# Performance work log

Measured on AMD Instinct MI355X. Metric: run time of the kernel, lower is better.

## Reference

```python
import jax, jax.numpy as jnp
import numpy as np

B, S, E, NH = 2, 2048, 512, 4
DH = E // NH  # 128
KSZ = 4      # causal conv kernel size


def setup_inputs() -> dict:
    key = jax.random.key(0)
    ks = jax.random.split(key, 12)
    hw_std = (2.0 / 5.0 / DH) ** 0.5
    return {
        "x": jax.random.normal(ks[0], (B, S, E), jnp.float32),
        "W_up": jax.random.normal(ks[1], (2 * E, E), jnp.float32) * 0.02,
        "Wq": jax.random.normal(ks[2], (NH, DH, DH), jnp.float32) * hw_std,
        "Wk": jax.random.normal(ks[3], (NH, DH, DH), jnp.float32) * hw_std,
        "Wv": jax.random.normal(ks[4], (NH, DH, DH), jnp.float32) * hw_std,
        "conv_w": jax.random.normal(ks[5], (E, E, KSZ), jnp.float32) * (1.0 / (E * KSZ) ** 0.5),
        "conv_b": jnp.zeros((E,), jnp.float32),
        "Wi": jax.random.normal(ks[6], (NH, 3 * E), jnp.float32) * 0.01,
        "bi": jax.random.normal(ks[7], (NH,), jnp.float32) * 0.1,
        "Wf": jax.random.normal(ks[8], (NH, 3 * E), jnp.float32) * 0.01,
        "bf": jax.random.normal(ks[9], (NH,), jnp.float32),
        "skip": jnp.ones((E,), jnp.float32),
        "W_down": jax.random.normal(ks[10], (E, E), jnp.float32) * 0.02,
        "b_down": jnp.zeros((E,), jnp.float32),
    }


def _headwise(u, W):
    # LinearHeadwiseExpand: x -> [B,S,NH,dh] @ [NH,od,dh]
    b, s, e = u.shape
    nh = W.shape[0]
    uh = u.reshape(b, s, nh, -1)
    return jnp.einsum('bshd,hod->bsho', uh, W).reshape(b, s, e)


def reference(x, W_up, Wq, Wk, Wv, conv_w, conv_b, Wi, bi, Wf, bf, skip, W_down, b_down):
    b, s, e = x.shape
    nh = Wq.shape[0]
    dh = e // nh
    eps = 1e-6

    x_inner = x @ W_up.T                        # [B,S,2E]
    x_mlstm, z = jnp.split(x_inner, 2, axis=-1)

    # causal conv1d: left-pad kernel_size-1, trim implicit via padding spec
    xc = jnp.transpose(x_mlstm, (0, 2, 1))      # [B,E,S]
    conv = jax.lax.conv_general_dilated(
        xc, conv_w, window_strides=(1,), padding=[(KSZ - 1, 0)],
        dimension_numbers=('NCH', 'OIH', 'NCH')) + conv_b[None, :, None]
    x_conv_act = jax.nn.silu(jnp.transpose(conv, (0, 2, 1)))  # [B,S,E]

    q = _headwise(x_conv_act, Wq)
    k = _headwise(x_conv_act, Wk)
    v = _headwise(x_mlstm, Wv)

    gate_in = jnp.concatenate([q, k, v], axis=-1)           # [B,S,3E]
    igate = jnp.transpose(gate_in @ Wi.T + bi, (0, 2, 1))   # [B,NH,S]
    fgate = jnp.transpose(gate_in @ Wf.T + bf, (0, 2, 1))   # [B,NH,S]

    qh = jnp.transpose(q.reshape(b, s, nh, dh), (0, 2, 1, 3))  # [B,NH,S,DH]
    kh = jnp.transpose(k.reshape(b, s, nh, dh), (0, 2, 1, 3))
    vh = jnp.transpose(v.reshape(b, s, nh, dh), (0, 2, 1, 3))

    # log-space cumulative forget-gate D matrix
    log_fg = jax.nn.log_sigmoid(fgate)                      # [B,NH,S]
    lfc = jnp.cumsum(log_fg, axis=-1)                       # [B,NH,S]
    log_fg_mat = lfc[..., :, None] - lfc[..., None, :]      # [B,NH,S,S]
    mask = jnp.tril(jnp.ones((s, s), bool))
    log_fg_mat = jnp.where(mask, log_fg_mat, -jnp.inf)
    log_D = log_fg_mat + igate[..., None, :]                # + igate[j]

    max_log_D = jnp.max(log_D, axis=-1, keepdims=True)      # rowwise stabilize
    Dm = jnp.exp(log_D - max_log_D)

    qk = jnp.einsum('bhsd,bhtd->bhst', qh, kh) / (dh ** 0.5)
    C = qk * Dm
    normalizer = jnp.maximum(jnp.abs(jnp.sum(C, axis=-1, keepdims=True)),
                             jnp.exp(-max_log_D))
    Cn = C / (normalizer + eps)
    h = jnp.einsum('bhst,bhtd->bhsd', Cn, vh)               # [B,NH,S,DH]

    # MultiHeadLayerNorm = group_norm(num_groups=NH, no affine, eps=1e-5)
    ht = jnp.transpose(h, (0, 2, 1, 3))                     # [B,S,NH,DH]
    mean = jnp.mean(ht, axis=-1, keepdims=True)
    var = jnp.var(ht, axis=-1, keepdims=True)
    h_norm = ((ht - mean) / jnp.sqrt(var + 1e-5)).reshape(b, s, e)

    h_skip = h_norm + skip * x_conv_act
    h_state = h_skip * jax.nn.silu(z)
    return h_state @ W_down.T + b_down
```

## Files before the change

### kernel.cpp

```cpp
#include <hip/hip_runtime.h>
#include <hip/hip_bf16.h>
#include <math.h>

typedef __hip_bfloat16 bf16;
typedef unsigned short ushort_t;
typedef __bf16 v8bf __attribute__((ext_vector_type(8)));
typedef float v4f __attribute__((ext_vector_type(4)));

#define B_   2
#define S_   2048
#define E_   512
#define NH_  4
#define DH_  128
#define NIN_ 14
#define NSPLIT_ 4

__device__ inline ushort_t f2bf(float f) {
  union { float f; unsigned u; } v; v.f = f;
  unsigned r = (v.u + 0x7FFFu + ((v.u >> 16) & 1u)) >> 16;
  return (ushort_t)r;
}
__device__ inline float bf2f(ushort_t u) {
  union { unsigned uu; float ff; } c; c.uu = (unsigned)u << 16; return c.ff;
}

struct CvtArgs {
  const void* src[NIN_];
  float* dst[NIN_];
  ushort_t* bdst[NIN_];
  int sz[NIN_];
};

__global__ __launch_bounds__(256) void convert_all(CvtArgs a, const unsigned* modew) {
  const bool isbf = (*modew == 0x3F803F80u);
  const int t = blockIdx.y;
  const int n = a.sz[t];
  const int base = blockIdx.x * 1024 + threadIdx.x;
  const float* sf = (const float*)a.src[t];
  const bf16*  sb = (const bf16*)a.src[t];
  const ushort_t* su = (const ushort_t*)a.src[t];
  float* d = a.dst[t];
  ushort_t* bd = a.bdst[t];
#pragma unroll
  for (int k = 0; k < 4; ++k) {
    int idx = base + k * 256;
    if (idx < n) {
      float f = isbf ? __bfloat162float(sb[idx]) : sf[idx];
      if (d)  d[idx] = f;
      if (bd) bd[idx] = isbf ? su[idx] : f2bf(f);
    }
  }
}

__global__ __launch_bounds__(256) void conv_repack(
    const void* __restrict__ src, ushort_t* __restrict__ Wt, const unsigned* __restrict__ modew)
{
  const bool isbf = (*modew == 0x3F803F80u);
  int idx = blockIdx.x * 256 + threadIdx.x;
  if (idx < E_ * E_ * 4) {
    int k = idx & 3, i = (idx >> 2) & (E_ - 1), o = idx >> 11;
    ushort_t v;
    if (isbf) v = ((const ushort_t*)src)[idx];
    else      v = f2bf(((const float*)src)[idx]);
    Wt[((size_t)k * E_ + o) * E_ + i] = v;
  }
}

__global__ __launch_bounds__(256) void gates_repack(
    const void* __restrict__ wi, const void* __restrict__ wf,
    ushort_t* __restrict__ Wgh, ushort_t* __restrict__ Wgl,
    const unsigned* __restrict__ modew)
{
  const bool isbf = (*modew == 0x3F803F80u);
  int idx = blockIdx.x * 256 + threadIdx.x;
  if (idx < 16 * 3 * E_) {
    int row = idx / (3 * E_), col = idx % (3 * E_);
    float w = 0.f;
    if (row < 4)      w = isbf ? bf2f(((const ushort_t*)wi)[row * 3 * E_ + col])
                               : ((const float*)wi)[row * 3 * E_ + col];
    else if (row < 8) w = isbf ? bf2f(((const ushort_t*)wf)[(row - 4) * 3 * E_ + col])
                               : ((const float*)wf)[(row - 4) * 3 * E_ + col];
    ushort_t hi = f2bf(w);
    Wgh[idx] = hi;
    Wgl[idx] = f2bf(w - bf2f(hi));
  }
}

template <int NT, bool HAS_BIAS, bool OUT_BF16, bool OUT_LO, bool OUT_DUAL>
__global__ __launch_bounds__(128, 4) void gemm2(
    const ushort_t* __restrict__ A, int lda,
    const ushort_t* __restrict__ Bm, int ldb,
    const float* __restrict__ bias,
    ushort_t* __restrict__ Cb, ushort_t* __restrict__ Cl,
    void* __restrict__ Cd, int ldc,
    int M, int K, const unsigned* __restrict__ modew)
{
  const int nm = M >> 6;
  const int m0 = (blockIdx.x % nm) << 6;
  const int n0 = (blockIdx.x / nm) * (NT * 16);
  const int tid = threadIdx.x;
  const int wv = tid >> 6, lane = tid & 63;
  const int ln15 = lane & 15, quad = lane >> 4;
  const int mA = m0 + wv * 16 + ln15;
  const int mB = mA + 32;
  v4f accA[NT], accB[NT];
#pragma unroll
  for (int i = 0; i < NT; ++i) { accA[i] = (v4f){0,0,0,0}; accB[i] = (v4f){0,0,0,0}; }
  const ushort_t* arowA = A + (size_t)mA * lda + quad * 8;
  const ushort_t* arowB = A + (size_t)mB * lda + quad * 8;
  const ushort_t* brow = Bm + (size_t)(n0 + ln15) * ldb + quad * 8;
  for (int k0 = 0; k0 < K; k0 += 32) {
    v8bf aA = *(const v8bf*)(arowA + k0);
    v8bf aB = *(const v8bf*)(arowB + k0);
#pragma unroll
    for (int nt = 0; nt < NT; ++nt) {
      v8bf b = *(const v8bf*)(brow + (size_t)nt * 16 * ldb + k0);
      accA[nt] = __builtin_amdgcn_mfma_f32_16x16x32_bf16(aA, b, accA[nt], 0, 0, 0);
      accB[nt] = __builtin_amdgcn_mfma_f32_16x16x32_bf16(aB, b, accB[nt], 0, 0, 0);
    }
  }
  bool obf = false;
  if (OUT_DUAL) obf = (*modew == 0x3F803F80u);
#pragma unroll
  for (int half = 0; half < 2; ++half) {
    const v4f* acc = half ? accB : accA;
#pragma unroll
    for (int nt = 0; nt < NT; ++nt) {
#pragma unroll
      for (int rr = 0; rr < 4; ++rr) {
        int m = m0 + wv * 16 + half * 32 + quad * 4 + rr;
        int n = n0 + nt * 16 + ln15;
        float c = acc[nt][rr];
        if (HAS_BIAS) c += bias[n];
        size_t off = (size_t)m * ldc + n;
        if (OUT_BF16) {
          ushort_t hi = f2bf(c);
          Cb[off] = hi;
          if (OUT_LO) Cl[off] = f2bf(c - bf2f(hi));
        }
        if (OUT_DUAL) {
          if (obf) ((bf16*)Cd)[off] = __float2bfloat16(c);
          else     ((float*)Cd)[off] = c;
        }
      }
    }
  }
}

__global__ __launch_bounds__(256, 2) void conv_lds2(
    const ushort_t* __restrict__ xhi,
    const ushort_t* __restrict__ xlo,
    const ushort_t* __restrict__ Wt,
    const float* __restrict__ cb,
    float* __restrict__ xca,
    ushort_t* __restrict__ xcab)
{
  const int m0 = (blockIdx.x & 63) << 6;
  const int n0 = (blockIdx.x >> 6) << 6;
  const int tid = threadIdx.x;
  const int wv = tid >> 6;
  const int lane = tid & 63;
  const int ln15 = lane & 15, quad = lane >> 4;
  const bool boundary = (m0 & (S_ - 1)) == 0;

  constexpr int LP = 132;
  __shared__ ushort_t Ab[2][68 * LP];

  int srow[17], scol[17], sstr[17];
#pragma unroll
  for (int j = 0; j < 17; ++j) {
    int idx = j * 256 + tid;
    sstr[j] = idx / 2176;
    int rem = idx - sstr[j] * 2176;
    srow[j] = rem >> 5;
    scol[j] = (rem & 31) << 2;
  }
  ushort4 sreg[17];
  auto stage_load = [&](int c) {
#pragma unroll
    for (int j = 0; j < 17; ++j) {
      const ushort_t* src = sstr[j] ? xlo : xhi;
      sreg[j] = *(const ushort4*)(src + (ptrdiff_t)(m0 - 4 + srow[j]) * (2 * E_)
                                  + c * 128 + scol[j]);
    }
    if (boundary) {
#pragma unroll
      for (int j = 0; j < 17; ++j)
        if (srow[j] < 4) sreg[j] = make_ushort4(0, 0, 0, 0);
    }
  };
  auto stage_write = [&]() {
#pragma unroll
    for (int j = 0; j < 17; ++j)
      *(ushort4*)&Ab[sstr[j]][srow[j] * LP + scol[j]] = sreg[j];
  };

  v4f acc[4];
#pragma unroll
  for (int i = 0; i < 4; ++i) acc[i] = (v4f){0, 0, 0, 0};

  v8bf breg[16];
  auto loadB = [&](int c) {
    const ushort_t* bw = Wt + (size_t)(n0 + wv * 16 + ln15) * E_ + c * 128 + quad * 8;
#pragma unroll
    for (int t = 0; t < 4; ++t)
#pragma unroll
      for (int k0 = 0; k0 < 4; ++k0)
        breg[t * 4 + k0] = *(const v8bf*)(bw + (size_t)t * E_ * E_ + k0 * 32);
  };
  auto compute = [&]() {
#pragma unroll
    for (int t = 0; t < 4; ++t) {
#pragma unroll
      for (int k0 = 0; k0 < 4; ++k0) {
#pragma unroll
        for (int rt = 0; rt < 4; ++rt) {
          const int ro = (rt * 16 + ln15 + t + 1) * LP + k0 * 32 + quad * 8;
          v8bf a1 = *(const v8bf*)&Ab[0][ro];
          v8bf a2 = *(const v8bf*)&Ab[1][ro];
          acc[rt] = __builtin_amdgcn_mfma_f32_16x16x32_bf16(a1, breg[t * 4 + k0], acc[rt], 0, 0, 0);
          acc[rt] = __builtin_amdgcn_mfma_f32_16x16x32_bf16(a2, breg[t * 4 + k0], acc[rt], 0, 0, 0);
        }
      }
    }
  };

  stage_load(0);
  stage_write();
  __syncthreads();
#pragma unroll
  for (int c = 0; c < 4; ++c) {
    if (c < 3) stage_load(c + 1);
    loadB(c);
    compute();
    if (c < 3) {
      __syncthreads();
      stage_write();
      __syncthreads();
    }
  }

  const int col = n0 + wv * 16 + ln15;
  const float cbv = cb[col];
#pragma unroll
  for (int rt = 0; rt < 4; ++rt) {
#pragma unroll
    for (int rr = 0; rr < 4; ++rr) {
      const int row = m0 + rt * 16 + quad * 4 + rr;
      float c = acc[rt][rr] + cbv;
      float r = c / (1.f + __expf(-c));
      const size_t off = (size_t)row * E_ + col;
      xca[off] = r;
      xcab[off] = f2bf(r);
    }
  }
}

__global__ __launch_bounds__(256) void qkv_mfma(
    const ushort_t* __restrict__ xcab,
    const ushort_t* __restrict__ xmb,
    const ushort_t* __restrict__ wqb, const ushort_t* __restrict__ wkb, const ushort_t* __restrict__ wvb,
    ushort_t* __restrict__ qb, ushort_t* __restrict__ kb, ushort_t* __restrict__ vb,
    ushort_t* __restrict__ vtb)
{
  const int type = blockIdx.y >> 2;
  const int h = blockIdx.y & 3;
  const int m0 = blockIdx.x << 6;
  const int tid = threadIdx.x;
  const int wv = tid >> 6, lane = tid & 63;
  const int ln15 = lane & 15, quad = lane >> 4;

  const ushort_t* Asrc = (type == 2) ? (xmb + h * DH_) : (xcab + h * DH_);
  const int lda = (type == 2) ? (2 * E_) : E_;
  const ushort_t* W = ((type == 0) ? wqb : (type == 1) ? wkb : wvb) + (size_t)h * DH_ * DH_;
  ushort_t* dst = (type == 0) ? qb : (type == 1) ? kb : vb;

  v4f acc[8];
#pragma unroll
  for (int i = 0; i < 8; ++i) acc[i] = (v4f){0.f, 0.f, 0.f, 0.f};

  const ushort_t* arow = Asrc + (size_t)(m0 + wv * 16 + ln15) * lda + quad * 8;
  const ushort_t* brow = W + (size_t)ln15 * DH_ + quad * 8;
#pragma unroll
  for (int c = 0; c < 4; ++c) {
    v8bf a = *(const v8bf*)(arow + c * 32);
#pragma unroll
    for (int nt = 0; nt < 8; ++nt) {
      v8bf b = *(const v8bf*)(brow + (size_t)nt * 16 * DH_ + c * 32);
      acc[nt] = __builtin_amdgcn_mfma_f32_16x16x32_bf16(a, b, acc[nt], 0, 0, 0);
    }
  }
  const int bb = m0 >> 11;
  const int s0 = (m0 & (S_ - 1)) + wv * 16 + quad * 4;
#pragma unroll
  for (int nt = 0; nt < 8; ++nt) {
    ushort_t pk[4];
#pragma unroll
    for (int rr = 0; rr < 4; ++rr) {
      int m = m0 + wv * 16 + quad * 4 + rr;
      int s = m & (S_ - 1);
      int n = nt * 16 + ln15;
      ushort_t u = f2bf(acc[nt][rr]);
      pk[rr] = u;
      dst[((size_t)(bb * NH_ + h) * S_ + s) * DH_ + n] = u;
    }
    if (type == 2) {
      *(ushort4*)&vtb[((size_t)(bb * NH_ + h) * DH_ + nt * 16 + ln15) * S_ + s0] =
          make_ushort4(pk[0], pk[1], pk[2], pk[3]);
    }
  }
}

__global__ __launch_bounds__(64) void gates_mfma(
    const ushort_t* __restrict__ qb, const ushort_t* __restrict__ kb, const ushort_t* __restrict__ vb,
    const ushort_t* __restrict__ Wgh, const ushort_t* __restrict__ Wgl,
    const float* __restrict__ bi, const float* __restrict__ bfp,
    float* __restrict__ ig, float* __restrict__ fgo)
{
  const int m0 = blockIdx.x << 4;
  const int lane = threadIdx.x;
  const int ln15 = lane & 15, quad = lane >> 4;
  const int m = m0 + ln15;
  const int b = m >> 11, s = m & (S_ - 1);
  const size_t base0 = ((size_t)(b * NH_) * S_ + s) * DH_;

  v4f acc = (v4f){0.f, 0.f, 0.f, 0.f};
  const ushort_t* wh = Wgh + (size_t)ln15 * (3 * E_) + quad * 8;
  const ushort_t* wl = Wgl + (size_t)ln15 * (3 * E_) + quad * 8;
#pragma unroll
  for (int kk = 0; kk < 48; ++kk) {
    const int kg = kk * 32 + quad * 8;
    const int type = kg >> 9;
    const int h = (kg >> 7) & 3;
    const int d = kg & 127;
    const ushort_t* src = (type == 0) ? qb : (type == 1) ? kb : vb;
    v8bf a = *(const v8bf*)(src + base0 + (size_t)h * S_ * DH_ + d);
    v8bf bh2 = *(const v8bf*)(wh + kk * 32);
    v8bf bl2 = *(const v8bf*)(wl + kk * 32);
    acc = __builtin_amdgcn_mfma_f32_16x16x32_bf16(a, bh2, acc, 0, 0, 0);
    acc = __builtin_amdgcn_mfma_f32_16x16x32_bf16(a, bl2, acc, 0, 0, 0);
  }
  if (ln15 < 8) {
#pragma unroll
    for (int r = 0; r < 4; ++r) {
      int mm = m0 + quad * 4 + r;
      int bb2 = mm >> 11, ss = mm & (S_ - 1);
      if (ln15 < 4) ig [((size_t)(bb2 * NH_ + ln15)) * S_ + ss]       = acc[r] + bi[ln15];
      else          fgo[((size_t)(bb2 * NH_ + (ln15 - 4))) * S_ + ss] = acc[r] + bfp[ln15 - 4];
    }
  }
}

__global__ __launch_bounds__(256) void gate_scan(
    const float* __restrict__ fgv, const float* __restrict__ igv,
    float* __restrict__ lfc, float* __restrict__ gout, float* __restrict__ Mout)
{
  const int bh = blockIdx.x;
  const int tid = threadIdx.x;
  const float* f = fgv + (size_t)bh * S_;
  const float* ii = igv + (size_t)bh * S_;
  __shared__ float sb[256];
  float loc[8];
  float run = 0.f;
#pragma unroll
  for (int j = 0; j < 8; ++j) {
    float x = f[tid * 8 + j];
    float ls = (x >= 0.f) ? -log1pf(expf(-x)) : (x - log1pf(expf(x)));
    run += ls; loc[j] = run;
  }
  sb[tid] = run; __syncthreads();
  for (int off = 1; off < 256; off <<= 1) {
    float t = (tid >= off) ? sb[tid - off] : 0.f;
    __syncthreads();
    sb[tid] += t;
    __syncthreads();
  }
  float pre = (tid > 0) ? sb[tid - 1] : 0.f;
  float lv[8], gl[8];
  float mrun = -INFINITY;
#pragma unroll
  for (int j = 0; j < 8; ++j) {
    lv[j] = pre + loc[j];
    lfc[(size_t)bh * S_ + tid * 8 + j] = lv[j];
    float gg = ii[tid * 8 + j] - lv[j];
    gout[(size_t)bh * S_ + tid * 8 + j] = gg;
    mrun = fmaxf(mrun, gg); gl[j] = mrun;
  }
  __syncthreads();
  sb[tid] = mrun; __syncthreads();
  for (int off = 1; off < 256; off <<= 1) {
    float t = (tid >= off) ? sb[tid - off] : -INFINITY;
    __syncthreads();
    sb[tid] = fmaxf(sb[tid], t);
    __syncthreads();
  }
  float mpre = (tid > 0) ? sb[tid - 1] : -INFINITY;
#pragma unroll
  for (int j = 0; j < 8; ++j)
    Mout[(size_t)bh * S_ + tid * 8 + j] = fmaxf(mpre, gl[j]);
}

__global__ __launch_bounds__(256, 2) void attn_split(
    const ushort_t* __restrict__ qb, const ushort_t* __restrict__ kb,
    const ushort_t* __restrict__ vtb,
    const float* __restrict__ gv, const float* __restrict__ Mv,
    float* __restrict__ pbuf,
    float* __restrict__ pcs)
{
  const int bh = blockIdx.x & 7;
  const int j = (blockIdx.x >> 3) & 15;
  const int chunk = blockIdx.x >> 7;
  const ushort_t* q = qb + (size_t)bh * S_ * DH_;
  const ushort_t* k = kb + (size_t)bh * S_ * DH_;
  const ushort_t* vt = vtb + (size_t)bh * DH_ * S_;
  const float* gp = gv + (size_t)bh * S_;
  const float* Mp = Mv + (size_t)bh * S_;

  __shared__ ushort_t Ps[4][2][16][72];

  const int tid = threadIdx.x;
  const int wv = tid >> 6;
  const int lane = tid & 63;
  const int ln15 = lane & 15;
  const int quad = lane >> 4;
  const int rowLo = (j * 4 + wv) * 16;
  const int rowHi = rowLo + 1024;
  const float rs = 0.08838834764831845f;

  ushort_t (*PsLo)[72] = Ps[wv][0];
  ushort_t (*PsHi)[72] = Ps[wv][1];

  v8bf qfL[4], qfH[4];
#pragma unroll
  for (int c = 0; c < 4; ++c) {
    qfL[c] = *(const v8bf*)(q + (size_t)(rowLo + ln15) * DH_ + c * 32 + quad * 8);
    qfH[c] = *(const v8bf*)(q + (size_t)(rowHi + ln15) * DH_ + c * 32 + quad * 8);
  }
  float MrL[4], MrH[4];
#pragma unroll
  for (int r = 0; r < 4; ++r) {
    MrL[r] = Mp[rowLo + quad * 4 + r];
    MrH[r] = Mp[rowHi + quad * 4 + r];
  }

  v4f haccL[8], haccH[8];
#pragma unroll
  for (int i = 0; i < 8; ++i) { haccL[i] = (v4f){0,0,0,0}; haccH[i] = (v4f){0,0,0,0}; }
  float csL[4] = {0,0,0,0}, csH[4] = {0,0,0,0};

  const int NI = 17 + j;
  const int C = (NI + NSPLIT_ - 1) / NSPLIT_;
  const int it0 = chunk * C;
  const int it1 = (it0 + C < NI) ? (it0 + C) : NI;

  for (int it = it0; it < it1; ++it) {
    const int t0 = it << 6;
    const bool loIter = (t0 <= rowLo + 15);
#pragma unroll
    for (int tt = 0; tt < 4; ++tt) {
      const int tg0 = t0 + tt * 16;
      const bool hv = (tg0 <= rowHi + 15);
      const bool lv = (tg0 <= rowLo + 15);
      if (hv) {
        v4f sL = (v4f){0,0,0,0}, sH = (v4f){0,0,0,0};
        const ushort_t* kr = k + (size_t)(tg0 + ln15) * DH_ + quad * 8;
        if (lv) {
#pragma unroll
          for (int c = 0; c < 4; ++c) {
            v8bf kf = *(const v8bf*)(kr + c * 32);
            sH = __builtin_amdgcn_mfma_f32_16x16x32_bf16(qfH[c], kf, sH, 0, 0, 0);
            sL = __builtin_amdgcn_mfma_f32_16x16x32_bf16(qfL[c], kf, sL, 0, 0, 0);
          }
        } else {
#pragma unroll
          for (int c = 0; c < 4; ++c) {
            v8bf kf = *(const v8bf*)(kr + c * 32);
            sH = __builtin_amdgcn_mfma_f32_16x16x32_bf16(qfH[c], kf, sH, 0, 0, 0);
          }
        }
        const int tg = tg0 + ln15;
        const float gt = gp[tg];
#pragma unroll
        for (int r = 0; r < 4; ++r) {
          const int rowH = rowHi + quad * 4 + r;
          float p = sH[r] * rs * __expf(fminf(gt - MrH[r], 60.f));
          p = (tg <= rowH) ? p : 0.f;
          csH[r] += p;
          PsHi[quad * 4 + r][tt * 16 + ln15] = f2bf(p);
        }
        if (lv) {
#pragma unroll
          for (int r = 0; r < 4; ++r) {
            const int rowL = rowLo + quad * 4 + r;
            float p = sL[r] * rs * __expf(fminf(gt - MrL[r], 60.f));
            p = (tg <= rowL) ? p : 0.f;
            csL[r] += p;
            PsLo[quad * 4 + r][tt * 16 + ln15] = f2bf(p);
          }
        } else if (loIter) {
#pragma unroll
          for (int r = 0; r < 4; ++r) PsLo[quad * 4 + r][tt * 16 + ln15] = 0;
        }
      } else {
#pragma unroll
        for (int r = 0; r < 4; ++r) PsHi[quad * 4 + r][tt * 16 + ln15] = 0;
        if (loIter) {
#pragma unroll
          for (int r = 0; r < 4; ++r) PsLo[quad * 4 + r][tt * 16 + ln15] = 0;
        }
      }
    }
#pragma unroll
    for (int c2 = 0; c2 < 2; ++c2) {
      v8bf pfH = *(const v8bf*)&PsHi[ln15][c2 * 32 + quad * 8];
      if (loIter) {
        v8bf pfL = *(const v8bf*)&PsLo[ln15][c2 * 32 + quad * 8];
#pragma unroll
        for (int dt = 0; dt < 8; ++dt) {
          v8bf vf = *(const v8bf*)(vt + (size_t)(dt * 16 + ln15) * S_ + t0 + c2 * 32 + quad * 8);
          haccH[dt] = __builtin_amdgcn_mfma_f32_16x16x32_bf16(pfH, vf, haccH[dt], 0, 0, 0);
          haccL[dt] = __builtin_amdgcn_mfma_f32_16x16x32_bf16(pfL, vf, haccL[dt], 0, 0, 0);
        }
      } else {
#pragma unroll
        for (int dt = 0; dt < 8; ++dt) {
          v8bf vf = *(const v8bf*)(vt + (size_t)(dt * 16 + ln15) * S_ + t0 + c2 * 32 + quad * 8);
          haccH[dt] = __builtin_amdgcn_mfma_f32_16x16x32_bf16(pfH, vf, haccH[dt], 0, 0, 0);
        }
      }
    }
  }

#pragma unroll
  for (int r = 0; r < 4; ++r) {
    float a = csL[r], b2 = csH[r];
    a += __shfl_xor(a, 1, 64);  b2 += __shfl_xor(b2, 1, 64);
    a += __shfl_xor(a, 2, 64);  b2 += __shfl_xor(b2, 2, 64);
    a += __shfl_xor(a, 4, 64);  b2 += __shfl_xor(b2, 4, 64);
    a += __shfl_xor(a, 8, 64);  b2 += __shfl_xor(b2, 8, 64);
    csL[r] = a; csH[r] = b2;
  }
  const size_t slab = (size_t)(chunk * 8 + bh);
  if (ln15 == 0) {
#pragma unroll
    for (int r = 0; r < 4; ++r) {
      __builtin_nontemporal_store(csL[r], &pcs[slab * S_ + rowLo + quad * 4 + r]);
      __builtin_nontemporal_store(csH[r], &pcs[slab * S_ + rowHi + quad * 4 + r]);
    }
  }
#pragma unroll
  for (int dt = 0; dt < 8; ++dt) {
#pragma unroll
    for (int r = 0; r < 4; ++r) {
      __builtin_nontemporal_store(haccL[dt][r],
          &pbuf[(slab * S_ + rowLo + quad * 4 + r) * DH_ + dt * 16 + ln15]);
      __builtin_nontemporal_store(haccH[dt][r],
          &pbuf[(slab * S_ + rowHi + quad * 4 + r) * DH_ + dt * 16 + ln15]);
    }
  }
}

__global__ __launch_bounds__(256) void gn_fused(
    const float* __restrict__ pbuf, const float* __restrict__ pcs,
    const float* __restrict__ Mv, const float* __restrict__ lfcv,
    const float* __restrict__ xca,
    const ushort_t* __restrict__ xhib, const ushort_t* __restrict__ xlob,
    const float* __restrict__ skip,
    ushort_t* __restrict__ hsb)
{
  const int row = blockIdx.x;
  const int b = row >> 11, s2 = row & (S_ - 1);
  const int tid = threadIdx.x;
  const int hd = tid >> 6, lane = tid & 63;
  const int bh = b * NH_ + hd;

  float v0 = 0.f, v1 = 0.f, cs = 0.f;
#pragma unroll
  for (int c = 0; c < NSPLIT_; ++c) {
    const size_t base = ((size_t)(c * 8 + bh) * S_ + s2) * DH_;
    v0 += __builtin_nontemporal_load(&pbuf[base + lane]);
    v1 += __builtin_nontemporal_load(&pbuf[base + lane + 64]);
    cs += __builtin_nontemporal_load(&pcs[(size_t)(c * 8 + bh) * S_ + s2]);
  }
  const size_t off = (size_t)bh * S_ + s2;
  const float floorv = __expf(fminf(-(lfcv[off] + Mv[off]), 80.f));
  const float inv = 1.f / (fmaxf(fabsf(cs), floorv) + 1e-6f);
  v0 *= inv; v1 *= inv;

  float s = v0 + v1, q = v0 * v0 + v1 * v1;
  for (int o = 32; o > 0; o >>= 1) { s += __shfl_down(s, o, 64); q += __shfl_down(q, o, 64); }
  s = __shfl(s, 0, 64); q = __shfl(q, 0, 64);
  float mean = s * (1.f / 128.f);
  float var = q * (1.f / 128.f) - mean * mean;
  float rstd = rsqrtf(fmaxf(var, 0.f) + 1e-5f);
#pragma unroll
  for (int t2 = 0; t2 < 2; ++t2) {
    int e = hd * DH_ + lane + t2 * 64;
    float hv = (t2 == 0) ? v0 : v1;
    float hn = (hv - mean) * rstd;
    float hs = hn + skip[e] * xca[(size_t)row * E_ + e];
    size_t zoff = (size_t)row * (2 * E_) + E_ + e;
    float z = bf2f(xhib[zoff]) + bf2f(xlob[zoff]);
    float sz = z / (1.f + __expf(-z));
    hsb[(size_t)row * E_ + e] = f2bf(hs * sz);
  }
}

extern "C" void kernel_launch(void* const* d_in, const int* in_sizes, int n_in,
                              void* d_out, int out_size, void* d_ws, size_t ws_size,
                              hipStream_t stream) {
  (void)out_size; (void)ws_size; (void)n_in;
  const unsigned* modew = (const unsigned*)d_in[11];

  float* ws = (float*)d_ws;
  size_t cur = 0;
  auto allocf = [&](size_t n) { float* p = ws + cur; cur += (n + 3) & ~(size_t)3; return p; };
  auto allocb = [&](size_t n) { return (ushort_t*)allocf((n + 1) / 2); };

  const bool needf[NIN_] = {false,false,false,false,false,false,true,false,true,false,true,true,false,true};
  const bool needb[NIN_] = {true,true,true,true,true,false,false,false,false,false,false,false,true,false};

  float* cvf[NIN_];
  ushort_t* cvb[NIN_];
  CvtArgs ca;
  int maxsz = 0;
  for (int i = 0; i < NIN_; ++i) {
    cvf[i] = needf[i] ? allocf((size_t)in_sizes[i]) : nullptr;
    cvb[i] = needb[i] ? allocb((size_t)in_sizes[i]) : nullptr;
    ca.src[i] = d_in[i];
    ca.dst[i] = cvf[i];
    ca.bdst[i] = cvb[i];
    ca.sz[i] = in_sizes[i];
    if (in_sizes[i] > maxsz) maxsz = in_sizes[i];
  }

  const size_t nBS = (size_t)B_ * S_;
  ushort_t* Wtc      = allocb((size_t)4 * E_ * E_);
  ushort_t* Wgh      = allocb((size_t)16 * 3 * E_);
  ushort_t* Wgl      = allocb((size_t)16 * 3 * E_);
  ushort_t* x_innerb = allocb(nBS * 2 * E_);
  ushort_t* x_lob    = allocb(nBS * 2 * E_);
  float* xca         = allocf(nBS * E_);
  ushort_t* xcab     = allocb(nBS * E_);
  ushort_t* qbuf     = allocb(nBS * E_);
  ushort_t* kbuf     = allocb(nBS * E_);
  ushort_t* vbuf     = allocb(nBS * E_);
  ushort_t* vtbuf    = allocb(nBS * E_);
  float* ig      = allocf((size_t)B_ * NH_ * S_);
  float* fg      = allocf((size_t)B_ * NH_ * S_);
  float* lfc     = allocf((size_t)B_ * NH_ * S_);
  float* gbuf    = allocf((size_t)B_ * NH_ * S_);
  float* Mbuf    = allocf((size_t)B_ * NH_ * S_);
  float* pbuf    = allocf((size_t)NSPLIT_ * 8 * S_ * DH_);
  float* pcs     = allocf((size_t)NSPLIT_ * 8 * S_);
  ushort_t* hsb  = allocb(nBS * E_);

  convert_all<<<dim3((maxsz + 1023) / 1024, NIN_), 256, 0, stream>>>(ca, modew);
  conv_repack<<<dim3((E_ * E_ * 4 + 255) / 256), 256, 0, stream>>>(d_in[5], Wtc, modew);
  gates_repack<<<dim3((16 * 3 * E_ + 255) / 256), 256, 0, stream>>>(d_in[7], d_in[9], Wgh, Wgl, modew);
  gemm2<4, false, true, true, false><<<dim3(64 * (1024 / 64)), 128, 0, stream>>>(
      cvb[0], E_, cvb[1], E_, nullptr, x_innerb, x_lob, nullptr, 2 * E_, 4096, E_, modew);
  conv_lds2<<<dim3(64 * 8), 256, 0, stream>>>(x_innerb, x_lob, Wtc, cvf[6], xca, xcab);
  qkv_mfma<<<dim3(4096 / 64, 12), 256, 0, stream>>>(xcab, x_innerb, cvb[2], cvb[3], cvb[4],
                                                    qbuf, kbuf, vbuf, vtbuf);
  gates_mfma<<<dim3(4096 / 16), 64, 0, stream>>>(qbuf, kbuf, vbuf, Wgh, Wgl,
                                                 cvf[8], cvf[10], ig, fg);
  gate_scan<<<dim3(B_ * NH_), 256, 0, stream>>>(fg, ig, lfc, gbuf, Mbuf);
  attn_split<<<dim3(16 * NSPLIT_ * 8), 256, 0, stream>>>(
      qbuf, kbuf, vtbuf, gbuf, Mbuf, pbuf, pcs);
  gn_fused<<<dim3(4096), 256, 0, stream>>>(pbuf, pcs, Mbuf, lfc, xca, x_innerb, x_lob,
                                           cvf[11], hsb);
  gemm2<4, true, false, false, true><<<dim3(64 * (512 / 64)), 128, 0, stream>>>(
      hsb, E_, cvb[12], E_, cvf[13], nullptr, nullptr, d_out, E_, 4096, E_, modew);
}
```

Before: 295.2 us.

## Give each attention wave one row tile and add an unmasked fast path

The split attention kernel goes from 256 to 512 threads. Each of 8 waves now handles a single 16-row query tile, replacing the paired low/high tiles that shared K and V loads. The causal range is split evenly across the chunks. Fully unmasked 64-column blocks take a fast path that prefetches K and V fragments into registers and skips the causal select. The 1/sqrt(d) scale is folded into the exponent offset. This trades away K/V reuse between paired tiles for fewer live registers and less masking work, but may worsen load balance across blocks. The folded log-scale constant is slightly inexact.

```diff
diff --git a/kernel.cpp b/kernel.cpp
--- a/kernel.cpp
+++ b/kernel.cpp
@@ -400,7 +400,7 @@
     Mout[(size_t)bh * S_ + tid * 8 + j] = fmaxf(mpre, gl[j]);
 }
 
-__global__ __launch_bounds__(256, 2) void attn_split(
+__global__ __launch_bounds__(512, 2) void attn_split(
     const ushort_t* __restrict__ qb, const ushort_t* __restrict__ kb,
     const ushort_t* __restrict__ vtb,
     const float* __restrict__ gv, const float* __restrict__ Mv,
@@ -416,116 +416,112 @@
   const float* gp = gv + (size_t)bh * S_;
   const float* Mp = Mv + (size_t)bh * S_;
 
-  __shared__ ushort_t Ps[4][2][16][72];
+  __shared__ ushort_t Ps[8][16][72];
 
   const int tid = threadIdx.x;
   const int wv = tid >> 6;
   const int lane = tid & 63;
   const int ln15 = lane & 15;
   const int quad = lane >> 4;
-  const int rowLo = (j * 4 + wv) * 16;
-  const int rowHi = rowLo + 1024;
-  const float rs = 0.08838834764831845f;
-
-  ushort_t (*PsLo)[72] = Ps[wv][0];
-  ushort_t (*PsHi)[72] = Ps[wv][1];
-
-  v8bf qfL[4], qfH[4];
-#pragma unroll
-  for (int c = 0; c < 4; ++c) {
-    qfL[c] = *(const v8bf*)(q + (size_t)(rowLo + ln15) * DH_ + c * 32 + quad * 8);
-    qfH[c] = *(const v8bf*)(q + (size_t)(rowHi + ln15) * DH_ + c * 32 + quad * 8);
-  }
-  float MrL[4], MrH[4];
-#pragma unroll
-  for (int r = 0; r < 4; ++r) {
-    MrL[r] = Mp[rowLo + quad * 4 + r];
-    MrH[r] = Mp[rowHi + quad * 4 + r];
-  }
-
-  v4f haccL[8], haccH[8];
-#pragma unroll
-  for (int i = 0; i < 8; ++i) { haccL[i] = (v4f){0,0,0,0}; haccH[i] = (v4f){0,0,0,0}; }
-  float csL[4] = {0,0,0,0}, csH[4] = {0,0,0,0};
-
-  const int NI = 17 + j;
-  const int C = (NI + NSPLIT_ - 1) / NSPLIT_;
-  const int it0 = chunk * C;
-  const int it1 = (it0 + C < NI) ? (it0 + C) : NI;
+  const int tile = j * 8 + wv;
+  const int row0 = tile * 16;
+  const float lrs = 2.4245772f;
+
+  ushort_t (*Psw)[72] = Ps[wv];
+
+  v8bf qf[4];
+#pragma unroll
+  for (int c = 0; c < 4; ++c)
+    qf[c] = *(const v8bf*)(q + (size_t)(row0 + ln15) * DH_ + c * 32 + quad * 8);
+  float Mr[4];
+#pragma unroll
+  for (int r = 0; r < 4; ++r) Mr[r] = Mp[row0 + quad * 4 + r] + lrs;
+
+  v4f hacc[8];
+#pragma unroll
+  for (int i = 0; i < 8; ++i) hacc[i] = (v4f){0, 0, 0, 0};
+  float cs[4] = {0, 0, 0, 0};
+
+  const int NI = (row0 + 79) >> 6;
+  const int it0 = (chunk * NI) / NSPLIT_;
+  const int it1 = ((chunk + 1) * NI) / NSPLIT_;
 
   for (int it = it0; it < it1; ++it) {
     const int t0 = it << 6;
-    const bool loIter = (t0 <= rowLo + 15);
-#pragma unroll
-    for (int tt = 0; tt < 4; ++tt) {
-      const int tg0 = t0 + tt * 16;
-      const bool hv = (tg0 <= rowHi + 15);
-      const bool lv = (tg0 <= rowLo + 15);
-      if (hv) {
-        v4f sL = (v4f){0,0,0,0}, sH = (v4f){0,0,0,0};
-        const ushort_t* kr = k + (size_t)(tg0 + ln15) * DH_ + quad * 8;
-        if (lv) {
+    if (t0 + 63 <= row0) {
+      v8bf kf[4][4];
+#pragma unroll
+      for (int tt = 0; tt < 4; ++tt) {
+        const ushort_t* kr = k + (size_t)(t0 + tt * 16 + ln15) * DH_ + quad * 8;
+#pragma unroll
+        for (int c = 0; c < 4; ++c) kf[tt][c] = *(const v8bf*)(kr + c * 32);
+      }
+      v8bf vf0[8];
+#pragma unroll
+      for (int dt = 0; dt < 8; ++dt)
+        vf0[dt] = *(const v8bf*)(vt + (size_t)(dt * 16 + ln15) * S_ + t0 + quad * 8);
+#pragma unroll
+      for (int tt = 0; tt < 4; ++tt) {
+        v4f sS = (v4f){0, 0, 0, 0};
+#pragma unroll
+        for (int c = 0; c < 4; ++c)
+          sS = __builtin_amdgcn_mfma_f32_16x16x32_bf16(qf[c], kf[tt][c], sS, 0, 0, 0);
+        const float gt = gp[t0 + tt * 16 + ln15];
+#pragma unroll
+        for (int r = 0; r < 4; ++r) {
+          float p = sS[r] * __expf(fminf(gt - Mr[r], 60.f));
+          cs[r] += p;
+          Psw[quad * 4 + r][tt * 16 + ln15] = f2bf(p);
+        }
+      }
+      {
+        v8bf vf1[8];
+#pragma unroll
+        for (int dt = 0; dt < 8; ++dt)
+          vf1[dt] = *(const v8bf*)(vt + (size_t)(dt * 16 + ln15) * S_ + t0 + 32 + quad * 8);
+        v8bf pf0 = *(const v8bf*)&Psw[ln15][quad * 8];
+#pragma unroll
+        for (int dt = 0; dt < 8; ++dt)
+          hacc[dt] = __builtin_amdgcn_mfma_f32_16x16x32_bf16(pf0, vf0[dt], hacc[dt], 0, 0, 0);
+        v8bf pf1 = *(const v8bf*)&Psw[ln15][32 + quad * 8];
+#pragma unroll
+        for (int dt = 0; dt < 8; ++dt)
+          hacc[dt] = __builtin_amdgcn_mfma_f32_16x16x32_bf16(pf1, vf1[dt], hacc[dt], 0, 0, 0);
+      }
+    } else {
+#pragma unroll
+      for (int tt = 0; tt < 4; ++tt) {
+        const int tg0 = t0 + tt * 16;
+        if (tg0 <= row0 + 15) {
+          v4f sS = (v4f){0, 0, 0, 0};
+          const ushort_t* kr = k + (size_t)(tg0 + ln15) * DH_ + quad * 8;
 #pragma unroll
           for (int c = 0; c < 4; ++c) {
             v8bf kf = *(const v8bf*)(kr + c * 32);
-            sH = __builtin_amdgcn_mfma_f32_16x16x32_bf16(qfH[c], kf, sH, 0, 0, 0);
-            sL = __builtin_amdgcn_mfma_f32_16x16x32_bf16(qfL[c], kf, sL, 0, 0, 0);
+            sS = __builtin_amdgcn_mfma_f32_16x16x32_bf16(qf[c], kf, sS, 0, 0, 0);
+          }
+          const int tg = tg0 + ln15;
+          const float gt = gp[tg];
+#pragma unroll
+          for (int r = 0; r < 4; ++r) {
+            const int row = row0 + quad * 4 + r;
+            float p = sS[r] * __expf(fminf(gt - Mr[r], 60.f));
+            p = (tg <= row) ? p : 0.f;
+            cs[r] += p;
+            Psw[quad * 4 + r][tt * 16 + ln15] = f2bf(p);
           }
         } else {
 #pragma unroll
-          for (int c = 0; c < 4; ++c) {
-            v8bf kf = *(const v8bf*)(kr + c * 32);
-            sH = __builtin_amdgcn_mfma_f32_16x16x32_bf16(qfH[c], kf, sH, 0, 0, 0);
-          }
-        }
-        const int tg = tg0 + ln15;
-        const float gt = gp[tg];
-#pragma unroll
-        for (int r = 0; r < 4; ++r) {
-          const int rowH = rowHi + quad * 4 + r;
-          float p = sH[r] * rs * __expf(fminf(gt - MrH[r], 60.f));
-          p = (tg <= rowH) ? p : 0.f;
-          csH[r] += p;
-          PsHi[quad * 4 + r][tt * 16 + ln15] = f2bf(p);
-        }
-        if (lv) {
-#pragma unroll
-          for (int r = 0; r < 4; ++r) {
-            const int rowL = rowLo + quad * 4 + r;
-            float p = sL[r] * rs * __expf(fminf(gt - MrL[r], 60.f));
-            p = (tg <= rowL) ? p : 0.f;
-            csL[r] += p;
-            PsLo[quad * 4 + r][tt * 16 + ln15] = f2bf(p);
-          }
-        } else if (loIter) {
-#pragma unroll
-          for (int r = 0; r < 4; ++r) PsLo[quad * 4 + r][tt * 16 + ln15] = 0;
-        }
-      } else {
-#pragma unroll
-        for (int r = 0; r < 4; ++r) PsHi[quad * 4 + r][tt * 16 + ln15] = 0;
-        if (loIter) {
-#pragma unroll
-          for (int r = 0; r < 4; ++r) PsLo[quad * 4 + r][tt * 16 + ln15] = 0;
+          for (int r = 0; r < 4; ++r) Psw[quad * 4 + r][tt * 16 + ln15] = 0;
         }
       }
-    }
-#pragma unroll
-    for (int c2 = 0; c2 < 2; ++c2) {
-      v8bf pfH = *(const v8bf*)&PsHi[ln15][c2 * 32 + quad * 8];
-      if (loIter) {
-        v8bf pfL = *(const v8bf*)&PsLo[ln15][c2 * 32 + quad * 8];
+#pragma unroll
+      for (int c2 = 0; c2 < 2; ++c2) {
+        v8bf pf = *(const v8bf*)&Psw[ln15][c2 * 32 + quad * 8];
 #pragma unroll
         for (int dt = 0; dt < 8; ++dt) {
           v8bf vf = *(const v8bf*)(vt + (size_t)(dt * 16 + ln15) * S_ + t0 + c2 * 32 + quad * 8);
-          haccH[dt] = __builtin_amdgcn_mfma_f32_16x16x32_bf16(pfH, vf, haccH[dt], 0, 0, 0);
-          haccL[dt] = __builtin_amdgcn_mfma_f32_16x16x32_bf16(pfL, vf, haccL[dt], 0, 0, 0);
-        }
-      } else {
-#pragma unroll
-        for (int dt = 0; dt < 8; ++dt) {
-          v8bf vf = *(const v8bf*)(vt + (size_t)(dt * 16 + ln15) * S_ + t0 + c2 * 32 + quad * 8);
-          haccH[dt] = __builtin_amdgcn_mfma_f32_16x16x32_bf16(pfH, vf, haccH[dt], 0, 0, 0);
+          hacc[dt] = __builtin_amdgcn_mfma_f32_16x16x32_bf16(pf, vf, hacc[dt], 0, 0, 0);
         }
       }
     }
@@ -533,29 +529,25 @@
 
 #pragma unroll
   for (int r = 0; r < 4; ++r) {
-    float a = csL[r], b2 = csH[r];
-    a += __shfl_xor(a, 1, 64);  b2 += __shfl_xor(b2, 1, 64);
-    a += __shfl_xor(a, 2, 64);  b2 += __shfl_xor(b2, 2, 64);
-    a += __shfl_xor(a, 4, 64);  b2 += __shfl_xor(b2, 4, 64);
-    a += __shfl_xor(a, 8, 64);  b2 += __shfl_xor(b2, 8, 64);
-    csL[r] = a; csH[r] = b2;
+    float a = cs[r];
+    a += __shfl_xor(a, 1, 64);
+    a += __shfl_xor(a, 2, 64);
+    a += __shfl_xor(a, 4, 64);
+    a += __shfl_xor(a, 8, 64);
+    cs[r] = a;
   }
   const size_t slab = (size_t)(chunk * 8 + bh);
   if (ln15 == 0) {
 #pragma unroll
+    for (int r = 0; r < 4; ++r)
+      __builtin_nontemporal_store(cs[r], &pcs[slab * S_ + row0 + quad * 4 + r]);
+  }
+#pragma unroll
+  for (int dt = 0; dt < 8; ++dt) {
+#pragma unroll
     for (int r = 0; r < 4; ++r) {
-      __builtin_nontemporal_store(csL[r], &pcs[slab * S_ + rowLo + quad * 4 + r]);
-      __builtin_nontemporal_store(csH[r], &pcs[slab * S_ + rowHi + quad * 4 + r]);
-    }
-  }
-#pragma unroll
-  for (int dt = 0; dt < 8; ++dt) {
-#pragma unroll
-    for (int r = 0; r < 4; ++r) {
-      __builtin_nontemporal_store(haccL[dt][r],
-          &pbuf[(slab * S_ + rowLo + quad * 4 + r) * DH_ + dt * 16 + ln15]);
-      __builtin_nontemporal_store(haccH[dt][r],
-          &pbuf[(slab * S_ + rowHi + quad * 4 + r) * DH_ + dt * 16 + ln15]);
+      __builtin_nontemporal_store(hacc[dt][r],
+          &pbuf[(slab * S_ + row0 + quad * 4 + r) * DH_ + dt * 16 + ln15]);
     }
   }
 }
@@ -666,7 +658,7 @@
   gates_mfma<<<dim3(4096 / 16), 64, 0, stream>>>(qbuf, kbuf, vbuf, Wgh, Wgl,
                                                  cvf[8], cvf[10], ig, fg);
   gate_scan<<<dim3(B_ * NH_), 256, 0, stream>>>(fg, ig, lfc, gbuf, Mbuf);
-  attn_split<<<dim3(16 * NSPLIT_ * 8), 256, 0, stream>>>(
+  attn_split<<<dim3(16 * NSPLIT_ * 8), 512, 0, stream>>>(
       qbuf, kbuf, vtbuf, gbuf, Mbuf, pbuf, pcs);
   gn_fused<<<dim3(4096), 256, 0, stream>>>(pbuf, pcs, Mbuf, lfc, xca, x_innerb, x_lob,
                                            cvf[11], hsb);
```

After: 336.0 us. 13.8% more time.
